# Kernel tuning notes

Hardware: AMD Instinct MI355X
Metric: run time of the kernel (lower is better)

The kernel has to match this reference:

```python
import jax, jax.numpy as jnp
import numpy as np

N, IN, H, C, E = 50000, 128, 2, 64, 800000
HC = H * C  # 128
NEG_SLOPE = 0.2
EPS_GN = 1e-5


def setup_inputs() -> dict:
    key = jax.random.key(0)
    ks = jax.random.split(key, 32)
    r = lambda i, shape: jax.random.normal(ks[i], shape, dtype=jnp.float32) * 0.1
    inp = {
        'x': jax.random.normal(ks[0], (N, IN), dtype=jnp.float32),
        'edge_index': jax.random.randint(ks[1], (2, E), 0, N, dtype=jnp.int64),
        # conv 0: in=128 -> heads*emb=128
        'Wl0': r(2, (IN, HC)), 'bl0': jnp.zeros((HC,), jnp.float32),
        'Wr0': r(3, (IN, HC)), 'br0': jnp.zeros((HC,), jnp.float32),
        'att0': r(4, (H, C)), 'bias0': jnp.zeros((HC,), jnp.float32),
        # conv 1: in=128 -> 128
        'Wl1': r(5, (HC, HC)), 'bl1': jnp.zeros((HC,), jnp.float32),
        'Wr1': r(6, (HC, HC)), 'br1': jnp.zeros((HC,), jnp.float32),
        'att1': r(7, (H, C)), 'bias1': jnp.zeros((HC,), jnp.float32),
        # GraphNorm params (weight, bias, mean_scale)
        'g0': jnp.ones((HC,), jnp.float32), 'be0': jnp.zeros((HC,), jnp.float32), 'ms0': jnp.ones((HC,), jnp.float32),
        'g1': jnp.ones((HC,), jnp.float32), 'be1': jnp.zeros((HC,), jnp.float32), 'ms1': jnp.ones((HC,), jnp.float32),
        # MLP head
        'W1': r(8, (HC, C)), 'b1': jnp.zeros((C,), jnp.float32),
        'W2': r(9, (C, 2)), 'b2': jnp.zeros((2,), jnp.float32),
    }
    return inp


def gatv2_conv(x, src, dst, Wl, bl, Wr, br, att, bias):
    # PyG GATv2Conv: separate source/target transforms, edge attention, segment softmax
    xl = (x @ Wl + bl).reshape(N, H, C)  # source features
    xr = (x @ Wr + br).reshape(N, H, C)  # target features
    m = jax.nn.leaky_relu(xl[src] + xr[dst], NEG_SLOPE)  # [Etot, H, C]
    e = jnp.einsum('ehc,hc->eh', m, att)                  # [Etot, H]
    emax = jax.ops.segment_max(e, dst, num_segments=N)    # stable softmax per dst
    ex = jnp.exp(e - emax[dst])
    denom = jax.ops.segment_sum(ex, dst, num_segments=N)
    alpha = ex / (denom[dst] + 1e-16)
    out = jax.ops.segment_sum(xl[src] * alpha[:, :, None], dst, num_segments=N)
    return out.reshape(N, HC) + bias


def graph_norm(x, gamma, beta, mean_scale):
    # PyG GraphNorm with batch=None (single graph)
    mean = x.mean(axis=0)
    out = x - mean_scale * mean
    var = (out * out).mean(axis=0)
    return gamma * out / jnp.sqrt(var + EPS_GN) + beta


def reference(x, edge_index, Wl0, bl0, Wr0, br0, att0, bias0,
              Wl1, bl1, Wr1, br1, att1, bias1,
              g0, be0, ms0, g1, be1, ms1, W1, b1, W2, b2):
    loop = jnp.arange(N, dtype=edge_index.dtype)
    src = jnp.concatenate([edge_index[0], loop])  # add_self_loops=True
    dst = jnp.concatenate([edge_index[1], loop])
    # layer 0 (conv + GraphNorm + ReLU)
    h = jax.nn.relu(graph_norm(gatv2_conv(x, src, dst, Wl0, bl0, Wr0, br0, att0, bias0), g0, be0, ms0))
    # layer 1
    h = jax.nn.relu(graph_norm(gatv2_conv(h, src, dst, Wl1, bl1, Wr1, br1, att1, bias1), g1, be1, ms1))
    # dropout is identity in eval mode
    h = jax.nn.relu(h @ W1 + b1)
    return h @ W2 + b2
```

## Files before the change

kernel.cpp:

```cpp
#include <hip/hip_runtime.h>
#include <hip/hip_bf16.h>

#define N_NODES 50000
#define NE      800000
#define NETOT   (NE + N_NODES)
#define NEG     0.2f
#define NBUCK   196
#define NSEG    64
#define SEGCAP  128
#define NCTR    (NBUCK * NSEG)

typedef unsigned short u16;
typedef unsigned int   u32;
typedef __attribute__((ext_vector_type(8))) short bf16x8;
typedef __attribute__((ext_vector_type(4))) float f32x4;

__device__ __forceinline__ float b2f(u16 v) {
    union { float f; u32 u; } c; c.u = ((u32)v) << 16; return c.f;
}
__device__ __forceinline__ u16 f2b(float f) {
    union { float f; u32 u; } c; c.f = f;
    u32 r = c.u + 0x7FFF + ((c.u >> 16) & 1);
    return (u16)(r >> 16);
}
__device__ __forceinline__ float ldf(const void* p, int i, int fmt) {
    return fmt ? b2f(((const u16*)p)[i]) : ((const float*)p)[i];
}

__global__ void probe_fmt(const u32* __restrict__ w, int stride, int* __restrict__ dst) {
    int l = threadIdx.x;
    u32 v = w[l * stride + 1];
    u32 e = (v >> 7) & 0xFF;
    int ok = (e >= 100 && e <= 140) ? 1 : 0;
    unsigned long long m = __ballot(ok);
    if (l == 0) dst[0] = (__popcll(m) >= 48) ? 1 : 0;
}

__global__ void detect_i64(const int* __restrict__ ei, int* __restrict__ flag) {
    int l = threadIdx.x;
    int idx = (l * 25000) | 1;
    int v = ei[idx];
    unsigned long long nz = __ballot(v != 0);
    if (l == 0) flag[2] = (nz == 0ULL) ? 1 : 0;
}

__global__ void zero_bcnt(int* __restrict__ bcnt, int* __restrict__ flag) {
    int i = blockIdx.x * 256 + threadIdx.x;
    if (i < NCTR) bcnt[i] = 0;
    if (i == 0) flag[1] = 0;
}

__global__ void bin_a(const int* __restrict__ ei, const int* __restrict__ flag,
                      int* __restrict__ bcnt, uint2* __restrict__ pairs) {
    int e = blockIdx.x * 256 + threadIdx.x;
    if (e >= NE) return;
    int f = flag[2];
    int s, d;
    if (f) { s = ei[2 * e]; d = ei[2 * (NE + e)]; }
    else   { s = ei[e];     d = ei[NE + e]; }
    int idx = (d >> 8) * NSEG + (blockIdx.x & (NSEG - 1));
    int pos = atomicAdd(&bcnt[idx], 1);
    if (pos < SEGCAP) pairs[(size_t)idx * SEGCAP + pos] = make_uint2((u32)s, (u32)d);
}

__global__ void bucket_scan(const int* __restrict__ bcnt, int* __restrict__ bbase,
                            int* __restrict__ indptr) {
    __shared__ int sh[256];
    int tid = threadIdx.x;
    int tot = 0;
    if (tid < NBUCK) {
        int nb0 = tid << 8;
        int nodes = min(256, N_NODES - nb0);
        int edges = 0;
        for (int seg = 0; seg < NSEG; ++seg)
            edges += min(bcnt[tid * NSEG + seg], SEGCAP);
        tot = edges + nodes;
    }
    sh[tid] = tot; __syncthreads();
    for (int off = 1; off < 256; off <<= 1) {
        int u = (tid >= off) ? sh[tid - off] : 0;
        __syncthreads();
        sh[tid] += u;
        __syncthreads();
    }
    if (tid < NBUCK) bbase[tid] = sh[tid] - tot;
    if (tid == 0) indptr[N_NODES] = sh[NBUCK - 1];
}

__global__ __launch_bounds__(256) void bin_b(const uint2* __restrict__ pairs,
        const int* __restrict__ bcnt, const int* __restrict__ bbase,
        int* __restrict__ indptr, int* __restrict__ srcs) {
    __shared__ int cnt[256];
    __shared__ int scn[256];
    __shared__ int msh[NSEG];
    int b = blockIdx.x, tid = threadIdx.x;
    int nb0 = b << 8;
    int nodesHere = min(256, N_NODES - nb0);
    if (tid < NSEG) msh[tid] = min(bcnt[b * NSEG + tid], SEGCAP);
    cnt[tid] = (tid < nodesHere) ? 1 : 0;
    __syncthreads();
    const uint2* bp = pairs + (size_t)b * NSEG * SEGCAP;
    for (int t = tid; t < NSEG * SEGCAP; t += 256) {
        int seg = t >> 7, i = t & (SEGCAP - 1);
        if (i < msh[seg]) {
            int d = (int)bp[t].y;
            atomicAdd(&cnt[d - nb0], 1);
        }
    }
    __syncthreads();
    int v = cnt[tid];
    scn[tid] = v; __syncthreads();
    for (int off = 1; off < 256; off <<= 1) {
        int u = (tid >= off) ? scn[tid - off] : 0;
        __syncthreads();
        scn[tid] += u;
        __syncthreads();
    }
    int myoff = bbase[b] + scn[tid] - v;
    if (tid < nodesHere) indptr[nb0 + tid] = myoff;
    __syncthreads();
    cnt[tid] = myoff;
    __syncthreads();
    if (tid < nodesHere) {
        int pos = atomicAdd(&cnt[tid], 1);
        srcs[pos] = nb0 + tid;
    }
    for (int t = tid; t < NSEG * SEGCAP; t += 256) {
        int seg = t >> 7, i = t & (SEGCAP - 1);
        if (i < msh[seg]) {
            uint2 p = bp[t];
            int pos = atomicAdd(&cnt[(int)p.y - nb0], 1);
            srcs[pos] = (int)p.x;
        }
    }
}

#define LDP 136
__global__ __launch_bounds__(256) void gemm_xf(const void* __restrict__ inp,
        const int* __restrict__ fin, const int* __restrict__ fw,
        const void* __restrict__ Wl, const void* __restrict__ bl,
        const void* __restrict__ Wr, const void* __restrict__ br,
        const float* __restrict__ nscale, const float* __restrict__ nshift,
        u16* __restrict__ XL, u16* __restrict__ XR) {
    __shared__ u16 As16[64 * LDP];
    __shared__ u16 Bs16[64 * LDP];
    __shared__ float Sc[128], Sh[128];
    int fi = fin[0], fb = fw[0];
    int by = blockIdx.y;
    const void* W  = (by < 2) ? Wl : Wr;
    const void* bi = (by < 2) ? bl : br;
    u16* dst       = (by < 2) ? XL : XR;
    int jb = (by & 1) * 64;
    int n0 = blockIdx.x * 64;
    int tid = threadIdx.x;
    bool donorm = (nscale != nullptr);
    if (donorm) {
        if (tid < 128) { Sc[tid] = nscale[tid]; Sh[tid] = nshift[tid]; }
        __syncthreads();
    }
    if (fi) {
        for (int t = tid; t < 64 * 16; t += 256) {
            int node = t >> 4, c8 = (t & 15) << 3;
            int n = n0 + node;
            bf16x8 v = {0,0,0,0,0,0,0,0};
            if (n < N_NODES) v = *(const bf16x8*)((const u16*)inp + (size_t)n * 128 + c8);
            *(bf16x8*)&As16[node * LDP + c8] = v;
        }
    } else {
        for (int t = tid; t < 64 * 32; t += 256) {
            int node = t >> 5, c4 = (t & 31) << 2;
            int n = n0 + node;
            float4 v = {0.f, 0.f, 0.f, 0.f};
            if (n < N_NODES) v = *(const float4*)((const float*)inp + (size_t)n * 128 + c4);
            if (donorm) {
                v.x = fmaxf(v.x * Sc[c4]     + Sh[c4],     0.f);
                v.y = fmaxf(v.y * Sc[c4 + 1] + Sh[c4 + 1], 0.f);
                v.z = fmaxf(v.z * Sc[c4 + 2] + Sh[c4 + 2], 0.f);
                v.w = fmaxf(v.w * Sc[c4 + 3] + Sh[c4 + 3], 0.f);
            }
            ushort4 h;
            h.x = f2b(v.x); h.y = f2b(v.y); h.z = f2b(v.z); h.w = f2b(v.w);
            *(ushort4*)&As16[node * LDP + c4] = h;
        }
    }
    if (fb) {
        for (int t = tid; t < 128 * 8; t += 256) {
            int k = t >> 3, j8 = (t & 7) << 3;
            bf16x8 v = *(const bf16x8*)((const u16*)W + k * 128 + jb + j8);
            #pragma unroll
            for (int q = 0; q < 8; ++q) Bs16[(j8 + q) * LDP + k] = (u16)v[q];
        }
    } else {
        for (int t = tid; t < 128 * 16; t += 256) {
            int k = t >> 4, j4 = (t & 15) << 2;
            float4 v = *(const float4*)((const float*)W + k * 128 + jb + j4);
            Bs16[(j4 + 0) * LDP + k] = f2b(v.x);
            Bs16[(j4 + 1) * LDP + k] = f2b(v.y);
            Bs16[(j4 + 2) * LDP + k] = f2b(v.z);
            Bs16[(j4 + 3) * LDP + k] = f2b(v.w);
        }
    }
    __syncthreads();

    int wv = tid >> 6, lane = tid & 63;
    int quad = lane >> 4, r = lane & 15;
    int m0 = wv * 16;
    f32x4 acc[4] = {{0.f,0.f,0.f,0.f},{0.f,0.f,0.f,0.f},
                    {0.f,0.f,0.f,0.f},{0.f,0.f,0.f,0.f}};
    #pragma unroll
    for (int ks = 0; ks < 4; ++ks) {
        int ko = ks * 32 + quad * 8;
        bf16x8 af = *(const bf16x8*)&As16[(m0 + r) * LDP + ko];
        #pragma unroll
        for (int t = 0; t < 4; ++t) {
            bf16x8 bfr = *(const bf16x8*)&Bs16[(t * 16 + r) * LDP + ko];
            acc[t] = __builtin_amdgcn_mfma_f32_16x16x32_bf16(af, bfr, acc[t], 0, 0, 0);
        }
    }
    #pragma unroll
    for (int t = 0; t < 4; ++t) {
        int j = jb + t * 16 + r;
        float bj = ldf(bi, j, fb);
        #pragma unroll
        for (int reg = 0; reg < 4; ++reg) {
            int node = n0 + m0 + quad * 4 + reg;
            if (node < N_NODES) dst[node * 128 + j] = f2b(acc[t][reg] + bj);
        }
    }
}

__global__ __launch_bounds__(64) void agg_kernel(const u16* __restrict__ XL,
        const u16* __restrict__ XR, const void* __restrict__ att,
        const int* __restrict__ fmt,
        const int* __restrict__ indptr, const int* __restrict__ srcs,
        float4* __restrict__ OUT4) {
    int lane = threadIdx.x;
    int n = blockIdx.x;
    int eh = lane >> 5, q = lane & 31;
    int fb = fmt[0];
    ushort4 xrv = *(const ushort4*)(XR + (size_t)n * 128 + q * 4);
    float xr0 = b2f(xrv.x), xr1 = b2f(xrv.y), xr2 = b2f(xrv.z), xr3 = b2f(xrv.w);
    float a0 = ldf(att, 4 * q,     fb);
    float a1 = ldf(att, 4 * q + 1, fb);
    float a2 = ldf(att, 4 * q + 2, fb);
    float a3 = ldf(att, 4 * q + 3, fb);
    int beg = indptr[n], end = indptr[n + 1];
    float acc0 = 0.f, acc1 = 0.f, acc2 = 0.f, acc3 = 0.f, dsum = 0.f;
    int nit = (end - beg + 1) >> 1;
    for (int it = 0; it < nit; ++it) {
        int i = beg + 2 * it + eh;
        bool valid = (i < end);
        int s = valid ? srcs[i] : 0;
        ushort4 xlv = *(const ushort4*)(XL + (size_t)s * 128 + q * 4);
        float x0 = b2f(xlv.x), x1 = b2f(xlv.y), x2 = b2f(xlv.z), x3 = b2f(xlv.w);
        float t0 = x0 + xr0; t0 = fmaxf(t0, 0.f) + NEG * fminf(t0, 0.f);
        float t1 = x1 + xr1; t1 = fmaxf(t1, 0.f) + NEG * fminf(t1, 0.f);
        float t2 = x2 + xr2; t2 = fmaxf(t2, 0.f) + NEG * fminf(t2, 0.f);
        float t3 = x3 + xr3; t3 = fmaxf(t3, 0.f) + NEG * fminf(t3, 0.f);
        float p = t0 * a0;
        p = fmaf(t1, a1, p); p = fmaf(t2, a2, p); p = fmaf(t3, a3, p);
        p += __shfl_xor(p, 1);
        p += __shfl_xor(p, 2);
        p += __shfl_xor(p, 4);
        p += __shfl_xor(p, 8);
        float w = valid ? __expf(fminf(p, 60.f)) : 0.f;
        acc0 = fmaf(w, x0, acc0); acc1 = fmaf(w, x1, acc1);
        acc2 = fmaf(w, x2, acc2); acc3 = fmaf(w, x3, acc3);
        dsum += w;
    }
    acc0 += __shfl_xor(acc0, 32);
    acc1 += __shfl_xor(acc1, 32);
    acc2 += __shfl_xor(acc2, 32);
    acc3 += __shfl_xor(acc3, 32);
    dsum += __shfl_xor(dsum, 32);
    if (eh == 0) {
        float inv = 1.f / (dsum + 1e-16f);
        float4 o; o.x = acc0 * inv; o.y = acc1 * inv; o.z = acc2 * inv; o.w = acc3 * inv;
        OUT4[(size_t)n * 32 + q] = o;
    }
}

__global__ void zero_small(float* __restrict__ p) { p[threadIdx.x] = 0.f; }

__global__ __launch_bounds__(256) void colstats(const float* __restrict__ OUT,
        const void* __restrict__ bias, const int* __restrict__ fmt,
        float* __restrict__ S1, float* __restrict__ S2) {
    __shared__ float sh1[256], sh2[256];
    int tid = threadIdx.x;
    int c = tid & 127, half = tid >> 7;
    float bf = ldf(bias, c, fmt[0]);
    float s1 = 0.f, s2 = 0.f;
    for (int r = blockIdx.x * 2 + half; r < N_NODES; r += gridDim.x * 2) {
        float t = OUT[r * 128 + c] + bf;
        s1 += t; s2 += t * t;
    }
    sh1[tid] = s1; sh2[tid] = s2; __syncthreads();
    if (tid < 128) {
        atomicAdd(&S1[c], sh1[tid] + sh1[tid + 128]);
        atomicAdd(&S2[c], sh2[tid] + sh2[tid + 128]);
    }
}

__global__ void finalize_norm(const float* __restrict__ S1, const float* __restrict__ S2,
        const void* __restrict__ gamma, const void* __restrict__ beta,
        const void* __restrict__ msc, const void* __restrict__ bias,
        const int* __restrict__ fmt,
        float* __restrict__ scaleA, float* __restrict__ shiftB) {
    int c = threadIdx.x;
    if (c >= 128) return;
    int fb = fmt[0];
    const float invN = 1.f / (float)N_NODES;
    float mean = S1[c] * invN;
    float ex2  = S2[c] * invN;
    float ms = ldf(msc, c, fb);
    float var = ex2 - 2.f * ms * mean * mean + ms * ms * mean * mean;
    float rstd = rsqrtf(var + 1e-5f);
    float A = ldf(gamma, c, fb) * rstd;
    scaleA[c] = A;
    shiftB[c] = ldf(beta, c, fb) - A * (ms * mean - ldf(bias, c, fb));
}

__global__ __launch_bounds__(256) void mlp_kernel(const float* __restrict__ H,
        const void* __restrict__ w1, const void* __restrict__ b1,
        const void* __restrict__ w2, const void* __restrict__ b2,
        const float* __restrict__ nscale, const float* __restrict__ nshift,
        const int* __restrict__ fmt,
        float* __restrict__ out) {
    __shared__ float W1s[128 * 64];
    __shared__ float W2s[128];
    __shared__ float b1s[64];
    __shared__ float Sc[128], Sh[128];
    int tid = threadIdx.x;
    int fb = fmt[0];
    if (fb) {
        for (int t = tid; t < 128 * 8; t += 256) {
            int row8 = t << 3;
            bf16x8 v = *(const bf16x8*)((const u16*)w1 + row8);
            #pragma unroll
            for (int q = 0; q < 8; ++q) W1s[row8 + q] = b2f((u16)v[q]);
        }
    } else {
        for (int t = tid; t < 128 * 64; t += 256) W1s[t] = ((const float*)w1)[t];
    }
    if (tid < 128) { W2s[tid] = ldf(w2, tid, fb); Sc[tid] = nscale[tid]; Sh[tid] = nshift[tid]; }
    if (tid < 64)  b1s[tid] = ldf(b1, tid, fb);
    __syncthreads();
    int n = blockIdx.x * 256 + tid;
    if (n >= N_NODES) return;
    float z[64];
    #pragma unroll
    for (int j = 0; j < 64; j++) z[j] = b1s[j];
    for (int kb = 0; kb < 128; kb += 16) {
        float h[16];
        #pragma unroll
        for (int t = 0; t < 4; t++) {
            float4 v = *(const float4*)&H[n * 128 + kb + t * 4];
            int c = kb + t * 4;
            h[4 * t]     = fmaxf(v.x * Sc[c]     + Sh[c],     0.f);
            h[4 * t + 1] = fmaxf(v.y * Sc[c + 1] + Sh[c + 1], 0.f);
            h[4 * t + 2] = fmaxf(v.z * Sc[c + 2] + Sh[c + 2], 0.f);
            h[4 * t + 3] = fmaxf(v.w * Sc[c + 3] + Sh[c + 3], 0.f);
        }
        #pragma unroll
        for (int i = 0; i < 16; i++) {
            float hv = h[i];
            const float* wrow = &W1s[(kb + i) * 64];
            #pragma unroll
            for (int j = 0; j < 64; j += 4) {
                const float4 w = *(const float4*)&wrow[j];
                z[j]     += hv * w.x;
                z[j + 1] += hv * w.y;
                z[j + 2] += hv * w.z;
                z[j + 3] += hv * w.w;
            }
        }
    }
    float o0 = ldf(b2, 0, fb), o1 = ldf(b2, 1, fb);
    #pragma unroll
    for (int j = 0; j < 64; j++) {
        float zr = fmaxf(z[j], 0.f);
        o0 += zr * W2s[j * 2];
        o1 += zr * W2s[j * 2 + 1];
    }
    if (o0 != o0) o0 = 12345.f;
    if (o1 != o1) o1 = 12345.f;
    float2 o; o.x = o0; o.y = o1;
    ((float2*)out)[n] = o;
}

extern "C" void kernel_launch(void* const* d_in, const int* in_sizes, int n_in,
                              void* d_out, int out_size, void* d_ws, size_t ws_size,
                              hipStream_t stream) {
    (void)in_sizes; (void)n_in; (void)out_size; (void)ws_size;
    const void* x    = d_in[0];
    const int*  ei   = (const int*)d_in[1];
    const void* Wl0  = d_in[2];
    const void* bl0  = d_in[3];
    const void* Wr0  = d_in[4];
    const void* br0  = d_in[5];
    const void* att0 = d_in[6];
    const void* bias0= d_in[7];
    const void* Wl1  = d_in[8];
    const void* bl1  = d_in[9];
    const void* Wr1  = d_in[10];
    const void* br1  = d_in[11];
    const void* att1 = d_in[12];
    const void* bias1= d_in[13];
    const void* g0   = d_in[14];
    const void* be0  = d_in[15];
    const void* ms0  = d_in[16];
    const void* g1   = d_in[17];
    const void* be1  = d_in[18];
    const void* ms1  = d_in[19];
    const void* W1   = d_in[20];
    const void* b1   = d_in[21];
    const void* W2   = d_in[22];
    const void* b2   = d_in[23];

    char* ws = (char*)d_ws;
    const size_t NF2 = (size_t)N_NODES * 128 * 2;
    const size_t NF4 = (size_t)N_NODES * 128 * 4;
    u16*   XLb = (u16*)(ws);
    u16*   XRb = (u16*)(ws + NF2);
    float* B2  = (float*)(ws + 2 * NF2);
    uint2* pairs = (uint2*)B2;
    char* small = ws + 2 * NF2 + NF4;
    float* S1     = (float*)(small);
    float* S2     = (float*)(small + 512);
    float* scaleA = (float*)(small + 1024);
    float* shiftB = (float*)(small + 1536);
    int*   flag   = (int*)(small + 2048);
    int*   bbase  = (int*)(small + 2112);
    int*   bcnt   = (int*)(small + 4096);
    int*   indptr = (int*)(small + 57344);
    int*   srcs   = indptr + (N_NODES + 64);

    const int* fX   = &flag[0];
    const int* fFP  = &flag[1];
    const int* fPar = &flag[3];

    probe_fmt<<<1, 64, 0, stream>>>((const u32*)x, 50000, &flag[0]);
    probe_fmt<<<1, 64, 0, stream>>>((const u32*)Wl0, 128, &flag[3]);
    detect_i64<<<1, 64, 0, stream>>>(ei, flag);
    zero_bcnt<<<(NCTR + 255) / 256, 256, 0, stream>>>(bcnt, flag);

    bin_a<<<(NE + 255) / 256, 256, 0, stream>>>(ei, flag, bcnt, pairs);
    bucket_scan<<<1, 256, 0, stream>>>(bcnt, bbase, indptr);
    bin_b<<<NBUCK, 256, 0, stream>>>(pairs, bcnt, bbase, indptr, srcs);

    dim3 ggemm((N_NODES + 63) / 64, 4);

    for (int layer = 0; layer < 2; ++layer) {
        const void* Wl = layer ? Wl1 : Wl0;  const void* bl = layer ? bl1 : bl0;
        const void* Wr = layer ? Wr1 : Wr0;  const void* br = layer ? br1 : br0;
        const void* at = layer ? att1 : att0;
        const void* bi = layer ? bias1 : bias0;
        const void* gm = layer ? g1 : g0;    const void* bt = layer ? be1 : be0;
        const void* mS = layer ? ms1 : ms0;
        const void* inp = layer ? (const void*)B2 : x;
        const int* fin  = layer ? fFP : fX;
        const float* ns = layer ? scaleA : nullptr;
        const float* nh = layer ? shiftB : nullptr;

        zero_small<<<1, 256, 0, stream>>>(S1);
        gemm_xf<<<ggemm, 256, 0, stream>>>(inp, fin, fPar, Wl, bl, Wr, br, ns, nh,
                                           XLb, XRb);
        agg_kernel<<<N_NODES, 64, 0, stream>>>(XLb, XRb, at, fPar, indptr, srcs,
                                               (float4*)B2);
        colstats<<<256, 256, 0, stream>>>(B2, bi, fPar, S1, S2);
        finalize_norm<<<1, 128, 0, stream>>>(S1, S2, gm, bt, mS, bi, fPar, scaleA, shiftB);
    }

    mlp_kernel<<<(N_NODES + 255) / 256, 256, 0, stream>>>(B2, W1, b1, W2, b2,
                                                          scaleA, shiftB, fPar,
                                                          (float*)d_out);
}
```

Before: 486.9 us.

## Widen aggregation gathers to 16B, pack two nodes per block, merge init kernels

The aggregation kernel now uses 16 lanes per edge, each loading 8 bf16 values with a uint4, so four edges are processed per wave iteration, and two nodes share a 128-thread block. This cuts the number of gather instructions and loop iterations per node. The three probe/detect kernels and the zeroing kernel are merged into one init kernel. The column-stat atomics and the zeroing launch are replaced by per-block partial sums that finalize_norm reduces serially over 256 blocks, trading a couple of launches for a short serial loop and more registers in aggregation.

```diff
diff --git a/kernel.cpp b/kernel.cpp
--- a/kernel.cpp
+++ b/kernel.cpp
@@ -26,28 +26,32 @@
 __device__ __forceinline__ float ldf(const void* p, int i, int fmt) {
     return fmt ? b2f(((const u16*)p)[i]) : ((const float*)p)[i];
 }
-
-__global__ void probe_fmt(const u32* __restrict__ w, int stride, int* __restrict__ dst) {
-    int l = threadIdx.x;
-    u32 v = w[l * stride + 1];
-    u32 e = (v >> 7) & 0xFF;
-    int ok = (e >= 100 && e <= 140) ? 1 : 0;
-    unsigned long long m = __ballot(ok);
-    if (l == 0) dst[0] = (__popcll(m) >= 48) ? 1 : 0;
-}
-
-__global__ void detect_i64(const int* __restrict__ ei, int* __restrict__ flag) {
-    int l = threadIdx.x;
-    int idx = (l * 25000) | 1;
-    int v = ei[idx];
-    unsigned long long nz = __ballot(v != 0);
-    if (l == 0) flag[2] = (nz == 0ULL) ? 1 : 0;
-}
-
-__global__ void zero_bcnt(int* __restrict__ bcnt, int* __restrict__ flag) {
-    int i = blockIdx.x * 256 + threadIdx.x;
-    if (i < NCTR) bcnt[i] = 0;
-    if (i == 0) flag[1] = 0;
+__device__ __forceinline__ float wlo(u32 w) { return __uint_as_float(w << 16); }
+__device__ __forceinline__ float whi(u32 w) { return __uint_as_float(w & 0xffff0000u); }
+
+__global__ void init_all(const u32* __restrict__ xw, const u32* __restrict__ w0,
+                         const int* __restrict__ ei,
+                         int* __restrict__ flag, int* __restrict__ bcnt) {
+    int g = blockIdx.x * 256 + threadIdx.x;
+    if (g < NCTR) bcnt[g] = 0;
+    if (blockIdx.x == 0) {
+        int wv = threadIdx.x >> 6, l = threadIdx.x & 63;
+        if (wv == 0) {
+            u32 v = xw[l * 50000 + 1];
+            u32 e = (v >> 7) & 0xFF;
+            unsigned long long m = __ballot(e >= 100 && e <= 140);
+            if (l == 0) { flag[0] = (__popcll(m) >= 48) ? 1 : 0; flag[1] = 0; }
+        } else if (wv == 1) {
+            u32 v = w0[l * 128 + 1];
+            u32 e = (v >> 7) & 0xFF;
+            unsigned long long m = __ballot(e >= 100 && e <= 140);
+            if (l == 0) flag[3] = (__popcll(m) >= 48) ? 1 : 0;
+        } else if (wv == 2) {
+            int v = ei[(l * 25000) | 1];
+            unsigned long long nz = __ballot(v != 0);
+            if (l == 0) flag[2] = (nz == 0ULL) ? 1 : 0;
+        }
+    }
 }
 
 __global__ void bin_a(const int* __restrict__ ei, const int* __restrict__ flag,
@@ -229,62 +233,80 @@
     }
 }
 
-__global__ __launch_bounds__(64) void agg_kernel(const u16* __restrict__ XL,
-        const u16* __restrict__ XR, const void* __restrict__ att,
+__global__ __launch_bounds__(128) void agg_kernel(const uint4* __restrict__ XL4,
+        const uint4* __restrict__ XR4, const void* __restrict__ att,
         const int* __restrict__ fmt,
         const int* __restrict__ indptr, const int* __restrict__ srcs,
         float4* __restrict__ OUT4) {
-    int lane = threadIdx.x;
-    int n = blockIdx.x;
-    int eh = lane >> 5, q = lane & 31;
+    int wv = threadIdx.x >> 6;
+    int lane = threadIdx.x & 63;
+    int n = blockIdx.x * 2 + wv;
+    if (n >= N_NODES) return;
+    int eh = lane >> 4, q = lane & 15;
     int fb = fmt[0];
-    ushort4 xrv = *(const ushort4*)(XR + (size_t)n * 128 + q * 4);
-    float xr0 = b2f(xrv.x), xr1 = b2f(xrv.y), xr2 = b2f(xrv.z), xr3 = b2f(xrv.w);
-    float a0 = ldf(att, 4 * q,     fb);
-    float a1 = ldf(att, 4 * q + 1, fb);
-    float a2 = ldf(att, 4 * q + 2, fb);
-    float a3 = ldf(att, 4 * q + 3, fb);
+    uint4 xr = XR4[(size_t)n * 16 + q];
+    float xr0 = wlo(xr.x), xr1 = whi(xr.x), xr2 = wlo(xr.y), xr3 = whi(xr.y);
+    float xr4 = wlo(xr.z), xr5 = whi(xr.z), xr6 = wlo(xr.w), xr7 = whi(xr.w);
+    float a0 = ldf(att, 8 * q,     fb), a1 = ldf(att, 8 * q + 1, fb);
+    float a2 = ldf(att, 8 * q + 2, fb), a3 = ldf(att, 8 * q + 3, fb);
+    float a4 = ldf(att, 8 * q + 4, fb), a5 = ldf(att, 8 * q + 5, fb);
+    float a6 = ldf(att, 8 * q + 6, fb), a7 = ldf(att, 8 * q + 7, fb);
     int beg = indptr[n], end = indptr[n + 1];
-    float acc0 = 0.f, acc1 = 0.f, acc2 = 0.f, acc3 = 0.f, dsum = 0.f;
-    int nit = (end - beg + 1) >> 1;
+    float c0 = 0.f, c1 = 0.f, c2 = 0.f, c3 = 0.f;
+    float c4 = 0.f, c5 = 0.f, c6 = 0.f, c7 = 0.f, dsum = 0.f;
+    int nit = (end - beg + 3) >> 2;
     for (int it = 0; it < nit; ++it) {
-        int i = beg + 2 * it + eh;
+        int i = beg + 4 * it + eh;
         bool valid = (i < end);
         int s = valid ? srcs[i] : 0;
-        ushort4 xlv = *(const ushort4*)(XL + (size_t)s * 128 + q * 4);
-        float x0 = b2f(xlv.x), x1 = b2f(xlv.y), x2 = b2f(xlv.z), x3 = b2f(xlv.w);
+        uint4 xl = XL4[(size_t)s * 16 + q];
+        float x0 = wlo(xl.x), x1 = whi(xl.x), x2 = wlo(xl.y), x3 = whi(xl.y);
+        float x4 = wlo(xl.z), x5 = whi(xl.z), x6 = wlo(xl.w), x7 = whi(xl.w);
         float t0 = x0 + xr0; t0 = fmaxf(t0, 0.f) + NEG * fminf(t0, 0.f);
         float t1 = x1 + xr1; t1 = fmaxf(t1, 0.f) + NEG * fminf(t1, 0.f);
         float t2 = x2 + xr2; t2 = fmaxf(t2, 0.f) + NEG * fminf(t2, 0.f);
         float t3 = x3 + xr3; t3 = fmaxf(t3, 0.f) + NEG * fminf(t3, 0.f);
+        float t4 = x4 + xr4; t4 = fmaxf(t4, 0.f) + NEG * fminf(t4, 0.f);
+        float t5 = x5 + xr5; t5 = fmaxf(t5, 0.f) + NEG * fminf(t5, 0.f);
+        float t6 = x6 + xr6; t6 = fmaxf(t6, 0.f) + NEG * fminf(t6, 0.f);
+        float t7 = x7 + xr7; t7 = fmaxf(t7, 0.f) + NEG * fminf(t7, 0.f);
         float p = t0 * a0;
         p = fmaf(t1, a1, p); p = fmaf(t2, a2, p); p = fmaf(t3, a3, p);
+        p = fmaf(t4, a4, p); p = fmaf(t5, a5, p); p = fmaf(t6, a6, p);
+        p = fmaf(t7, a7, p);
         p += __shfl_xor(p, 1);
         p += __shfl_xor(p, 2);
         p += __shfl_xor(p, 4);
-        p += __shfl_xor(p, 8);
         float w = valid ? __expf(fminf(p, 60.f)) : 0.f;
-        acc0 = fmaf(w, x0, acc0); acc1 = fmaf(w, x1, acc1);
-        acc2 = fmaf(w, x2, acc2); acc3 = fmaf(w, x3, acc3);
+        c0 = fmaf(w, x0, c0); c1 = fmaf(w, x1, c1);
+        c2 = fmaf(w, x2, c2); c3 = fmaf(w, x3, c3);
+        c4 = fmaf(w, x4, c4); c5 = fmaf(w, x5, c5);
+        c6 = fmaf(w, x6, c6); c7 = fmaf(w, x7, c7);
         dsum += w;
     }
-    acc0 += __shfl_xor(acc0, 32);
-    acc1 += __shfl_xor(acc1, 32);
-    acc2 += __shfl_xor(acc2, 32);
-    acc3 += __shfl_xor(acc3, 32);
+    c0 += __shfl_xor(c0, 16); c1 += __shfl_xor(c1, 16);
+    c2 += __shfl_xor(c2, 16); c3 += __shfl_xor(c3, 16);
+    c4 += __shfl_xor(c4, 16); c5 += __shfl_xor(c5, 16);
+    c6 += __shfl_xor(c6, 16); c7 += __shfl_xor(c7, 16);
+    dsum += __shfl_xor(dsum, 16);
+    c0 += __shfl_xor(c0, 32); c1 += __shfl_xor(c1, 32);
+    c2 += __shfl_xor(c2, 32); c3 += __shfl_xor(c3, 32);
+    c4 += __shfl_xor(c4, 32); c5 += __shfl_xor(c5, 32);
+    c6 += __shfl_xor(c6, 32); c7 += __shfl_xor(c7, 32);
     dsum += __shfl_xor(dsum, 32);
     if (eh == 0) {
         float inv = 1.f / (dsum + 1e-16f);
-        float4 o; o.x = acc0 * inv; o.y = acc1 * inv; o.z = acc2 * inv; o.w = acc3 * inv;
-        OUT4[(size_t)n * 32 + q] = o;
-    }
-}
-
-__global__ void zero_small(float* __restrict__ p) { p[threadIdx.x] = 0.f; }
+        float4 oA, oB;
+        oA.x = c0 * inv; oA.y = c1 * inv; oA.z = c2 * inv; oA.w = c3 * inv;
+        oB.x = c4 * inv; oB.y = c5 * inv; oB.z = c6 * inv; oB.w = c7 * inv;
+        OUT4[(size_t)n * 32 + 2 * q]     = oA;
+        OUT4[(size_t)n * 32 + 2 * q + 1] = oB;
+    }
+}
 
 __global__ __launch_bounds__(256) void colstats(const float* __restrict__ OUT,
         const void* __restrict__ bias, const int* __restrict__ fmt,
-        float* __restrict__ S1, float* __restrict__ S2) {
+        float* __restrict__ Sp1, float* __restrict__ Sp2) {
     __shared__ float sh1[256], sh2[256];
     int tid = threadIdx.x;
     int c = tid & 127, half = tid >> 7;
@@ -296,22 +318,27 @@
     }
     sh1[tid] = s1; sh2[tid] = s2; __syncthreads();
     if (tid < 128) {
-        atomicAdd(&S1[c], sh1[tid] + sh1[tid + 128]);
-        atomicAdd(&S2[c], sh2[tid] + sh2[tid + 128]);
-    }
-}
-
-__global__ void finalize_norm(const float* __restrict__ S1, const float* __restrict__ S2,
+        Sp1[blockIdx.x * 128 + tid] = sh1[tid] + sh1[tid + 128];
+        Sp2[blockIdx.x * 128 + tid] = sh2[tid] + sh2[tid + 128];
+    }
+}
+
+__global__ void finalize_norm(const float* __restrict__ Sp1, const float* __restrict__ Sp2,
         const void* __restrict__ gamma, const void* __restrict__ beta,
         const void* __restrict__ msc, const void* __restrict__ bias,
         const int* __restrict__ fmt,
         float* __restrict__ scaleA, float* __restrict__ shiftB) {
     int c = threadIdx.x;
     if (c >= 128) return;
+    float s1 = 0.f, s2 = 0.f;
+    for (int b = 0; b < 256; ++b) {
+        s1 += Sp1[b * 128 + c];
+        s2 += Sp2[b * 128 + c];
+    }
     int fb = fmt[0];
     const float invN = 1.f / (float)N_NODES;
-    float mean = S1[c] * invN;
-    float ex2  = S2[c] * invN;
+    float mean = s1 * invN;
+    float ex2  = s2 * invN;
     float ms = ldf(msc, c, fb);
     float var = ex2 - 2.f * ms * mean * mean + ms * ms * mean * mean;
     float rstd = rsqrtf(var + 1e-5f);
@@ -425,25 +452,22 @@
     float* B2  = (float*)(ws + 2 * NF2);
     uint2* pairs = (uint2*)B2;
     char* small = ws + 2 * NF2 + NF4;
-    float* S1     = (float*)(small);
-    float* S2     = (float*)(small + 512);
     float* scaleA = (float*)(small + 1024);
     float* shiftB = (float*)(small + 1536);
     int*   flag   = (int*)(small + 2048);
     int*   bbase  = (int*)(small + 2112);
-    int*   bcnt   = (int*)(small + 4096);
-    int*   indptr = (int*)(small + 57344);
+    float* Sp1    = (float*)(small + 4096);
+    float* Sp2    = (float*)(small + 4096 + 131072);
+    int*   bcnt   = (int*)(small + 4096 + 262144);
+    int*   indptr = (int*)(small + 4096 + 262144 + 50176);
     int*   srcs   = indptr + (N_NODES + 64);
 
     const int* fX   = &flag[0];
     const int* fFP  = &flag[1];
     const int* fPar = &flag[3];
 
-    probe_fmt<<<1, 64, 0, stream>>>((const u32*)x, 50000, &flag[0]);
-    probe_fmt<<<1, 64, 0, stream>>>((const u32*)Wl0, 128, &flag[3]);
-    detect_i64<<<1, 64, 0, stream>>>(ei, flag);
-    zero_bcnt<<<(NCTR + 255) / 256, 256, 0, stream>>>(bcnt, flag);
-
+    init_all<<<(NCTR + 255) / 256, 256, 0, stream>>>((const u32*)x, (const u32*)Wl0,
+                                                     ei, flag, bcnt);
     bin_a<<<(NE + 255) / 256, 256, 0, stream>>>(ei, flag, bcnt, pairs);
     bucket_scan<<<1, 256, 0, stream>>>(bcnt, bbase, indptr);
     bin_b<<<NBUCK, 256, 0, stream>>>(pairs, bcnt, bbase, indptr, srcs);
@@ -462,13 +486,15 @@
         const float* ns = layer ? scaleA : nullptr;
         const float* nh = layer ? shiftB : nullptr;
 
-        zero_small<<<1, 256, 0, stream>>>(S1);
         gemm_xf<<<ggemm, 256, 0, stream>>>(inp, fin, fPar, Wl, bl, Wr, br, ns, nh,
                                            XLb, XRb);
-        agg_kernel<<<N_NODES, 64, 0, stream>>>(XLb, XRb, at, fPar, indptr, srcs,
-                                               (float4*)B2);
-        colstats<<<256, 256, 0, stream>>>(B2, bi, fPar, S1, S2);
-        finalize_norm<<<1, 128, 0, stream>>>(S1, S2, gm, bt, mS, bi, fPar, scaleA, shiftB);
+        agg_kernel<<<(N_NODES + 1) / 2, 128, 0, stream>>>((const uint4*)XLb,
+                                                          (const uint4*)XRb,
+                                                          at, fPar, indptr, srcs,
+                                                          (float4*)B2);
+        colstats<<<256, 256, 0, stream>>>(B2, bi, fPar, Sp1, Sp2);
+        finalize_norm<<<1, 128, 0, stream>>>(Sp1, Sp2, gm, bt, mS, bi, fPar,
+                                             scaleA, shiftB);
     }
 
     mlp_kernel<<<(N_NODES + 255) / 256, 256, 0, stream>>>(B2, W1, b1, W2, b2,
```

After: 504.2 us. 1.04x slower.
